# Optimization experiments

Measured on AMD Instinct MI355X. Metric: run time of the kernel, lower is better.

The kernel has to match this reference:

```python
import jax, jax.numpy as jnp
import numpy as np

B, S, DM1, DM2, DK, DV = 8, 2048, 768, 768, 64, 64
EPS = 1e-5


def setup_inputs() -> dict:
    key = jax.random.key(0)
    ks = jax.random.split(key, 8)
    s1 = 1.0 / np.sqrt(DM1)
    s2 = 1.0 / np.sqrt(DM2)
    return {
        "x_1": jax.random.normal(ks[0], (B, S, DM1), jnp.float32),
        "x_2": jax.random.normal(ks[1], (B, S, DM2), jnp.float32),
        "Wq": jax.random.uniform(ks[2], (DM1, DK), jnp.float32, -s1, s1),
        "bq": jnp.zeros((DK,), jnp.float32),
        "Wk": jax.random.uniform(ks[3], (DM2, DK), jnp.float32, -s2, s2),
        "bk": jnp.zeros((DK,), jnp.float32),
        "Wv": jax.random.uniform(ks[4], (DM2, DV), jnp.float32, -s2, s2),
        "bv": jnp.zeros((DV,), jnp.float32),
        "gamma": jnp.ones((DV,), jnp.float32),
        "beta": jnp.zeros((DV,), jnp.float32),
    }


def reference(x_1, x_2, Wq, bq, Wk, bk, Wv, bv, gamma, beta):
    q = jnp.einsum("bsd,dk->bsk", x_1, Wq) + bq            # [B,S,DK]
    k = jnp.einsum("bsd,dk->bsk", x_2, Wk) + bk            # [B,S,DK]
    v = jnp.einsum("bsd,dv->bsv", x_2, Wv) + bv            # [B,S,DV]
    scores = jnp.einsum("bqk,bsk->bqs", q, k) / jnp.sqrt(jnp.float32(DK))
    w = jax.nn.softmax(scores, axis=-1)                    # [B,S,S]
    # reverse-weight transform (reverse=True)
    dim = w.shape[1]
    w = (1.0 - w) / (dim - 1)
    attn = jnp.einsum("bqs,bsv->bqv", w, v)                # [B,S,DV]
    mu = jnp.mean(attn, axis=-1, keepdims=True)
    var = jnp.var(attn, axis=-1, keepdims=True)
    out = (attn - mu) * jax.lax.rsqrt(var + EPS) * gamma + beta
    return out
```

## Files before the change

kernel.cpp:

```cpp
#include <hip/hip_runtime.h>
#include <hip/hip_bf16.h>

#define BATCH 8
#define SEQ   2048
#define DM    768
#define DD    64
#define BS (BATCH * SEQ)
#define SCALEQ 0.1803369380478f

typedef __bf16 bf16x8 __attribute__((ext_vector_type(8)));
typedef float  f32x4  __attribute__((ext_vector_type(4)));
typedef short  short8 __attribute__((ext_vector_type(8)));
typedef short  short4v __attribute__((ext_vector_type(4)));

#define MFMA16(a, b, c) __builtin_amdgcn_mfma_f32_16x16x32_bf16((a), (b), (c), 0, 0, 0)

__device__ __forceinline__ short f2bf(float x) {
    unsigned u = __builtin_bit_cast(unsigned, x);
    u = (u + 0x7fffu + ((u >> 16) & 1u)) >> 16;
    return (short)u;
}
__device__ __forceinline__ float bf2f(short s) {
    unsigned u = ((unsigned)(unsigned short)s) << 16;
    return __builtin_bit_cast(float, u);
}
__device__ __forceinline__ bf16x8 cvt8(float4 a, float4 b) {
    bf16x8 r;
    r[0] = (__bf16)a.x; r[1] = (__bf16)a.y; r[2] = (__bf16)a.z; r[3] = (__bf16)a.w;
    r[4] = (__bf16)b.x; r[5] = (__bf16)b.y; r[6] = (__bf16)b.z; r[7] = (__bf16)b.w;
    return r;
}

__global__ void prep_w_kernel(const float* __restrict__ Wq, const float* __restrict__ Wk,
                              const float* __restrict__ Wv, short* __restrict__ Wt,
                              float* __restrict__ C) {
    int idx = blockIdx.x * 256 + threadIdx.x;
    if (idx < BATCH * DD) C[idx] = 0.f;
    if (idx >= 3 * DM * DD) return;
    int m = idx / (DM * DD);
    int r = (idx % (DM * DD)) / DD;
    int c = idx % DD;
    const float* W = (m == 0) ? Wq : (m == 1) ? Wk : Wv;
    float scale = (m == 0) ? SCALEQ : 1.0f;
    Wt[m * DM * DD + c * DM + r] = f2bf(W[r * DD + c] * scale);
}

__global__ __launch_bounds__(256, 2) void proj_kernel(
        const float* __restrict__ x1, const float* __restrict__ x2,
        const short* __restrict__ Wt,
        const float* __restrict__ bq, const float* __restrict__ bk,
        const float* __restrict__ bv,
        short* __restrict__ Qs, short* __restrict__ Kb, short* __restrict__ Vtb,
        float* __restrict__ C) {
    const int tid = threadIdx.x, wave = tid >> 6, lane = tid & 63;
    const int quad = lane >> 4, l15 = lane & 15;
    const int kv = blockIdx.x & 1;
    const int r0 = (blockIdx.x >> 1) * 64;
    const float* x = kv ? x2 : x1;
    const short* W0 = Wt + (kv ? (size_t)(DM * DD) : 0);
    const short* W1 = Wt + 2 * (size_t)(DM * DD);

    const float* xp = x + (size_t)(r0 + wave * 16 + l15) * DM + quad * 8;
    const short* wp0[4];
    const short* wp1[4];
#pragma unroll
    for (int tn = 0; tn < 4; tn++) {
        wp0[tn] = W0 + (size_t)(tn * 16 + l15) * DM + quad * 8;
        wp1[tn] = W1 + (size_t)(tn * 16 + l15) * DM + quad * 8;
    }

    f32x4 acc0[4] = {}, acc1[4] = {};

    if (!kv) {
#pragma unroll
        for (int st = 0; st < 24; st++) {
            const int k0 = st * 32;
            float4 a = *(const float4*)(xp + k0);
            float4 b = *(const float4*)(xp + k0 + 4);
            bf16x8 af = cvt8(a, b);
#pragma unroll
            for (int tn = 0; tn < 4; tn++)
                acc0[tn] = MFMA16(af, *(const bf16x8*)(wp0[tn] + k0), acc0[tn]);
        }
#pragma unroll
        for (int tn = 0; tn < 4; tn++) {
            int v = tn * 16 + l15;
            float bb = bq[v] * SCALEQ;
#pragma unroll
            for (int r = 0; r < 4; r++)
                Qs[(size_t)(r0 + wave * 16 + quad * 4 + r) * DD + v] = f2bf(acc0[tn][r] + bb);
        }
    } else {
#pragma unroll
        for (int st = 0; st < 24; st++) {
            const int k0 = st * 32;
            float4 a = *(const float4*)(xp + k0);
            float4 b = *(const float4*)(xp + k0 + 4);
            bf16x8 af = cvt8(a, b);
#pragma unroll
            for (int tn = 0; tn < 4; tn++) {
                acc0[tn] = MFMA16(af, *(const bf16x8*)(wp0[tn] + k0), acc0[tn]);
                acc1[tn] = MFMA16(af, *(const bf16x8*)(wp1[tn] + k0), acc1[tn]);
            }
        }
#pragma unroll
        for (int tn = 0; tn < 4; tn++) {
            int v = tn * 16 + l15;
            float bb = bk[v];
#pragma unroll
            for (int r = 0; r < 4; r++)
                Kb[(size_t)(r0 + wave * 16 + quad * 4 + r) * DD + v] = f2bf(acc0[tn][r] + bb);
        }
        const int b = r0 / SEQ;
        const int sbase = (r0 % SEQ) + wave * 16 + quad * 4;
#pragma unroll
        for (int tn = 0; tn < 4; tn++) {
            int v = tn * 16 + l15;
            float bb = bv[v];
            short4v pk;
            float cs = 0.f;
#pragma unroll
            for (int r = 0; r < 4; r++) {
                pk[r] = f2bf(acc1[tn][r] + bb);
                cs += bf2f(pk[r]);
            }
            *(short4v*)(Vtb + ((size_t)b * DD + v) * SEQ + sbase) = pk;
            cs += __shfl_xor(cs, 16);
            cs += __shfl_xor(cs, 32);
            if (quad == 0) atomicAdd(&C[b * DD + v], cs);
        }
    }
}

#define PBS 72
__global__ __launch_bounds__(256, 2) void flash_kernel(
        const short* __restrict__ Q, const short* __restrict__ K,
        const short* __restrict__ Vt,
        short* __restrict__ Yp, float* __restrict__ Dp) {
    __shared__ __align__(16) short pbuf[4][64 * PBS];
    __shared__ float dl[4][64];
    const int tid  = threadIdx.x;
    const int wave = tid >> 6, lane = tid & 63, quad = lane >> 4, l15 = lane & 15;
    const int blk = blockIdx.x;
    const int b = blk & 7, qt = (blk >> 3) & 31, half = blk >> 8;
    const int q0 = qt * 64;

    bf16x8 qf[4][2];
#pragma unroll
    for (int qn = 0; qn < 4; qn++)
#pragma unroll
        for (int kc = 0; kc < 2; kc++)
            qf[qn][kc] = *(const bf16x8*)(Q + ((size_t)(b * SEQ + q0 + qn * 16 + l15)) * DD
                                          + kc * 32 + quad * 8);

    const short* Kbp = K  + (size_t)b * SEQ * DD;
    const short* Vbp = Vt + (size_t)b * DD * SEQ;
    f32x4 y[4][4] = {};
    float den[4] = {0.f, 0.f, 0.f, 0.f};
    short* pw = &pbuf[wave][0];

    const int s_begin = half * 1024 + wave * 256;
    for (int s0 = s_begin; s0 < s_begin + 256; s0 += 64) {
#pragma unroll
        for (int tn = 0; tn < 4; tn++) {
            const short* kf = Kbp + (size_t)(s0 + tn * 16 + l15) * DD + quad * 8;
            bf16x8 ka0 = *(const bf16x8*)kf;
            bf16x8 ka1 = *(const bf16x8*)(kf + 32);
#pragma unroll
            for (int qn = 0; qn < 4; qn++) {
                f32x4 z = {0.f, 0.f, 0.f, 0.f};
                z = MFMA16(ka0, qf[qn][0], z);
                z = MFMA16(ka1, qf[qn][1], z);
                short4v pk;
#pragma unroll
                for (int r = 0; r < 4; r++) {
                    float p = __builtin_amdgcn_exp2f(z[r]);
                    den[qn] += p;
                    pk[r] = f2bf(p);
                }
                *(short4v*)&pw[(qn * 16 + l15) * PBS + tn * 16 + quad * 4] = pk;
            }
        }
#pragma unroll
        for (int kc = 0; kc < 2; kc++) {
            bf16x8 pB[4];
#pragma unroll
            for (int qn = 0; qn < 4; qn++)
                pB[qn] = *(const bf16x8*)&pw[(qn * 16 + l15) * PBS + kc * 32 + quad * 8];
#pragma unroll
            for (int vn = 0; vn < 4; vn++) {
                bf16x8 va = *(const bf16x8*)(Vbp + (size_t)(vn * 16 + l15) * SEQ
                                             + s0 + kc * 32 + quad * 8);
#pragma unroll
                for (int qn = 0; qn < 4; qn++)
                    y[qn][vn] = MFMA16(va, pB[qn], y[qn][vn]);
            }
        }
    }
#pragma unroll
    for (int qn = 0; qn < 4; qn++) {
        den[qn] += __shfl_xor(den[qn], 16);
        den[qn] += __shfl_xor(den[qn], 32);
    }
#pragma unroll
    for (int qn = 0; qn < 4; qn++) {
#pragma unroll
        for (int vn = 0; vn < 4; vn++) {
            short4v pk;
#pragma unroll
            for (int r = 0; r < 4; r++) pk[r] = f2bf(y[qn][vn][r]);
            *(short4v*)&pw[(qn * 16 + l15) * PBS + vn * 16 + quad * 4] = pk;
        }
        if (quad == 0) dl[wave][qn * 16 + l15] = den[qn];
    }
    __syncthreads();
    {
        const int q = wave * 16 + l15;
        float D = dl[0][q] + dl[1][q] + dl[2][q] + dl[3][q];
        float ys[16];
#pragma unroll
        for (int j = 0; j < 16; j++) ys[j] = 0.f;
#pragma unroll
        for (int u = 0; u < 4; u++) {
#pragma unroll
            for (int h = 0; h < 2; h++) {
                bf16x8 t = *(const bf16x8*)&pbuf[u][q * PBS + quad * 16 + h * 8];
#pragma unroll
                for (int j = 0; j < 8; j++) ys[h * 8 + j] += (float)t[j];
            }
        }
        const size_t row = (size_t)b * SEQ + q0 + q;
        short8 o0, o1;
#pragma unroll
        for (int j = 0; j < 8; j++) { o0[j] = f2bf(ys[j]); o1[j] = f2bf(ys[8 + j]); }
        short* yout = Yp + ((size_t)half * BS + row) * DD + quad * 16;
        *(short8*)yout = o0;
        *(short8*)(yout + 8) = o1;
        if (quad == 0) Dp[half * BS + row] = D;
    }
}

__global__ __launch_bounds__(256) void reduce_ln_kernel(
        const short* __restrict__ Yp, const float* __restrict__ Dp,
        const float* __restrict__ C, const float* __restrict__ gamma,
        const float* __restrict__ beta, float* __restrict__ out) {
    const int row = blockIdx.x * 4 + (threadIdx.x >> 6);
    const int v = threadIdx.x & 63;
    const int b = row >> 11;
    float Y = bf2f(Yp[(size_t)row * DD + v]) + bf2f(Yp[((size_t)BS + row) * DD + v]);
    float D = Dp[row] + Dp[BS + row];
    float attn = (C[b * DD + v] - Y / D) * (1.0f / (float)(SEQ - 1));
    float msum = attn, ssum = attn * attn;
#pragma unroll
    for (int m = 1; m < 64; m <<= 1) {
        msum += __shfl_xor(msum, m);
        ssum += __shfl_xor(ssum, m);
    }
    float mu = msum * (1.0f / 64.0f);
    float var = ssum * (1.0f / 64.0f) - mu * mu;
    float rs = rsqrtf(var + 1e-5f);
    out[(size_t)row * DD + v] = (attn - mu) * rs * gamma[v] + beta[v];
}

extern "C" void kernel_launch(void* const* d_in, const int* in_sizes, int n_in,
                              void* d_out, int out_size, void* d_ws, size_t ws_size,
                              hipStream_t stream) {
    const float* x1    = (const float*)d_in[0];
    const float* x2    = (const float*)d_in[1];
    const float* Wq    = (const float*)d_in[2];
    const float* bq    = (const float*)d_in[3];
    const float* Wk    = (const float*)d_in[4];
    const float* bk    = (const float*)d_in[5];
    const float* Wv    = (const float*)d_in[6];
    const float* bv    = (const float*)d_in[7];
    const float* gamma = (const float*)d_in[8];
    const float* beta  = (const float*)d_in[9];
    float* out = (float*)d_out;

    char* ws = (char*)d_ws;
    short* Qs  = (short*)(ws);
    short* Kbf = (short*)(ws + (2ull << 20));
    short* Vtb = (short*)(ws + (4ull << 20));
    short* Wt  = (short*)(ws + (6ull << 20));
    float* Cc  = (float*)(ws + (6ull << 20) + 3 * DM * DD * 2);
    short* Yp  = (short*)(ws + (7ull << 20));
    float* Dp  = (float*)(ws + (11ull << 20));

    prep_w_kernel<<<576, 256, 0, stream>>>(Wq, Wk, Wv, Wt, Cc);
    proj_kernel<<<512, 256, 0, stream>>>(x1, x2, Wt, bq, bk, bv, Qs, Kbf, Vtb, Cc);
    flash_kernel<<<512, 256, 0, stream>>>(Qs, Kbf, Vtb, Yp, Dp);
    reduce_ln_kernel<<<BS / 4, 256, 0, stream>>>(Yp, Dp, Cc, gamma, beta, out);
}
```

Measured before the change: 203.6 us.

## Restructure projection kernel: per-wave weight columns in registers, one output per block

The projection kernel is reorganized so each block computes exactly one of Q, K or V, giving 768 blocks instead of 512. Each wave keeps its 16 weight columns resident in registers across the whole reduction, and all four 16-row groups of x are streamed through with next-step prefetching. This replaces the previous layout, where every wave reloaded weights from global memory and K/V blocks did double work. The balanced blocks should even out the load, but x is now read by every wave of a block and K/V blocks read x2 twice, with higher register pressure from the 24 cached weight fragments.

```diff
diff --git a/kernel.cpp b/kernel.cpp
--- a/kernel.cpp
+++ b/kernel.cpp
@@ -54,81 +54,81 @@
         float* __restrict__ C) {
     const int tid = threadIdx.x, wave = tid >> 6, lane = tid & 63;
     const int quad = lane >> 4, l15 = lane & 15;
-    const int kv = blockIdx.x & 1;
-    const int r0 = (blockIdx.x >> 1) * 64;
-    const float* x = kv ? x2 : x1;
-    const short* W0 = Wt + (kv ? (size_t)(DM * DD) : 0);
-    const short* W1 = Wt + 2 * (size_t)(DM * DD);
-
-    const float* xp = x + (size_t)(r0 + wave * 16 + l15) * DM + quad * 8;
-    const short* wp0[4];
-    const short* wp1[4];
-#pragma unroll
-    for (int tn = 0; tn < 4; tn++) {
-        wp0[tn] = W0 + (size_t)(tn * 16 + l15) * DM + quad * 8;
-        wp1[tn] = W1 + (size_t)(tn * 16 + l15) * DM + quad * 8;
-    }
-
-    f32x4 acc0[4] = {}, acc1[4] = {};
-
-    if (!kv) {
-#pragma unroll
-        for (int st = 0; st < 24; st++) {
-            const int k0 = st * 32;
-            float4 a = *(const float4*)(xp + k0);
-            float4 b = *(const float4*)(xp + k0 + 4);
-            bf16x8 af = cvt8(a, b);
-#pragma unroll
-            for (int tn = 0; tn < 4; tn++)
-                acc0[tn] = MFMA16(af, *(const bf16x8*)(wp0[tn] + k0), acc0[tn]);
-        }
-#pragma unroll
-        for (int tn = 0; tn < 4; tn++) {
-            int v = tn * 16 + l15;
-            float bb = bq[v] * SCALEQ;
+    const int typ = blockIdx.x % 3;
+    const int g   = blockIdx.x / 3;
+    const int r0  = g * 64;
+    const float* x = (typ == 0) ? x1 : x2;
+    const int col = wave * 16 + l15;
+
+    const short* wp = Wt + ((size_t)typ * DD + col) * DM + quad * 8;
+    bf16x8 wreg[24];
+#pragma unroll
+    for (int st = 0; st < 24; st++)
+        wreg[st] = *(const bf16x8*)(wp + st * 32);
+
+    const float* xp = x + (size_t)(r0 + l15) * DM + quad * 8;
+
+    f32x4 acc[4] = {};
+    float4 ca[4], cb[4];
+#pragma unroll
+    for (int rn = 0; rn < 4; rn++) {
+        const float* p = xp + (size_t)(rn * 16) * DM;
+        ca[rn] = *(const float4*)(p);
+        cb[rn] = *(const float4*)(p + 4);
+    }
+#pragma unroll
+    for (int st = 0; st < 24; st++) {
+        float4 na[4], nb[4];
+        if (st + 1 < 24) {
+#pragma unroll
+            for (int rn = 0; rn < 4; rn++) {
+                const float* p = xp + (size_t)(rn * 16) * DM + (st + 1) * 32;
+                na[rn] = *(const float4*)(p);
+                nb[rn] = *(const float4*)(p + 4);
+            }
+        }
+#pragma unroll
+        for (int rn = 0; rn < 4; rn++) {
+            bf16x8 af = cvt8(ca[rn], cb[rn]);
+            acc[rn] = MFMA16(af, wreg[st], acc[rn]);
+        }
+#pragma unroll
+        for (int rn = 0; rn < 4; rn++) { ca[rn] = na[rn]; cb[rn] = nb[rn]; }
+    }
+
+    if (typ == 0) {
+        float bb = bq[col] * SCALEQ;
+#pragma unroll
+        for (int rn = 0; rn < 4; rn++)
 #pragma unroll
             for (int r = 0; r < 4; r++)
-                Qs[(size_t)(r0 + wave * 16 + quad * 4 + r) * DD + v] = f2bf(acc0[tn][r] + bb);
-        }
+                Qs[(size_t)(r0 + rn * 16 + quad * 4 + r) * DD + col] = f2bf(acc[rn][r] + bb);
+    } else if (typ == 1) {
+        float bb = bk[col];
+#pragma unroll
+        for (int rn = 0; rn < 4; rn++)
+#pragma unroll
+            for (int r = 0; r < 4; r++)
+                Kb[(size_t)(r0 + rn * 16 + quad * 4 + r) * DD + col] = f2bf(acc[rn][r] + bb);
     } else {
-#pragma unroll
-        for (int st = 0; st < 24; st++) {
-            const int k0 = st * 32;
-            float4 a = *(const float4*)(xp + k0);
-            float4 b = *(const float4*)(xp + k0 + 4);
-            bf16x8 af = cvt8(a, b);
-#pragma unroll
-            for (int tn = 0; tn < 4; tn++) {
-                acc0[tn] = MFMA16(af, *(const bf16x8*)(wp0[tn] + k0), acc0[tn]);
-                acc1[tn] = MFMA16(af, *(const bf16x8*)(wp1[tn] + k0), acc1[tn]);
-            }
-        }
-#pragma unroll
-        for (int tn = 0; tn < 4; tn++) {
-            int v = tn * 16 + l15;
-            float bb = bk[v];
-#pragma unroll
-            for (int r = 0; r < 4; r++)
-                Kb[(size_t)(r0 + wave * 16 + quad * 4 + r) * DD + v] = f2bf(acc0[tn][r] + bb);
-        }
-        const int b = r0 / SEQ;
-        const int sbase = (r0 % SEQ) + wave * 16 + quad * 4;
-#pragma unroll
-        for (int tn = 0; tn < 4; tn++) {
-            int v = tn * 16 + l15;
-            float bb = bv[v];
+        const int b  = r0 >> 11;
+        const int sb = r0 & 2047;
+        float bb = bv[col];
+        short* vout = Vtb + ((size_t)b * DD + col) * SEQ + sb;
+        float cs = 0.f;
+#pragma unroll
+        for (int rn = 0; rn < 4; rn++) {
             short4v pk;
-            float cs = 0.f;
 #pragma unroll
             for (int r = 0; r < 4; r++) {
-                pk[r] = f2bf(acc1[tn][r] + bb);
+                pk[r] = f2bf(acc[rn][r] + bb);
                 cs += bf2f(pk[r]);
             }
-            *(short4v*)(Vtb + ((size_t)b * DD + v) * SEQ + sbase) = pk;
-            cs += __shfl_xor(cs, 16);
-            cs += __shfl_xor(cs, 32);
-            if (quad == 0) atomicAdd(&C[b * DD + v], cs);
-        }
+            *(short4v*)(vout + rn * 16 + quad * 4) = pk;
+        }
+        cs += __shfl_xor(cs, 16);
+        cs += __shfl_xor(cs, 32);
+        if (quad == 0) atomicAdd(&C[b * DD + col], cs);
     }
 }
 
@@ -287,7 +287,7 @@
     float* Dp  = (float*)(ws + (11ull << 20));
 
     prep_w_kernel<<<576, 256, 0, stream>>>(Wq, Wk, Wv, Wt, Cc);
-    proj_kernel<<<512, 256, 0, stream>>>(x1, x2, Wt, bq, bk, bv, Qs, Kbf, Vtb, Cc);
+    proj_kernel<<<768, 256, 0, stream>>>(x1, x2, Wt, bq, bk, bv, Qs, Kbf, Vtb, Cc);
     flash_kernel<<<512, 256, 0, stream>>>(Qs, Kbf, Vtb, Yp, Dp);
     reduce_ln_kernel<<<BS / 4, 256, 0, stream>>>(Yp, Dp, Cc, gamma, beta, out);
 }
```

After: 212.6 us. 4.4% more time.

## Stage projection inputs and weights through double-buffered LDS via global_load_lds

Applied to the files above, without the earlier changes.

The projection GEMM used to read x and the bf16 weights straight from global memory into registers, with each wave loading the weight tiles on its own. It now uses direct global-to-LDS async loads into a double buffer, with an XOR swizzle on the x tile, so the next K-slice can prefetch while MFMAs run on the current one. Weights loaded into LDS are shared by all four waves, which cuts redundant global traffic. In exchange the loop now has a __syncthreads per K-step, the 24-step loop is no longer unrolled, and LDS use grows, which could lower occupancy.

```diff
diff --git a/kernel.cpp b/kernel.cpp
--- a/kernel.cpp
+++ b/kernel.cpp
@@ -29,6 +29,11 @@
     r[0] = (__bf16)a.x; r[1] = (__bf16)a.y; r[2] = (__bf16)a.z; r[3] = (__bf16)a.w;
     r[4] = (__bf16)b.x; r[5] = (__bf16)b.y; r[6] = (__bf16)b.z; r[7] = (__bf16)b.w;
     return r;
+}
+__device__ __forceinline__ void gld16(const void* g, void* l) {
+    __builtin_amdgcn_global_load_lds(
+        (const __attribute__((address_space(1))) void*)g,
+        (__attribute__((address_space(3))) void*)l, 16, 0, 0);
 }
 
 __global__ void prep_w_kernel(const float* __restrict__ Wq, const float* __restrict__ Wk,
@@ -52,36 +57,59 @@
         const float* __restrict__ bv,
         short* __restrict__ Qs, short* __restrict__ Kb, short* __restrict__ Vtb,
         float* __restrict__ C) {
+    __shared__ __align__(16) float als[2][64 * 32];
+    __shared__ __align__(16) short wls[2][2][2048];
     const int tid = threadIdx.x, wave = tid >> 6, lane = tid & 63;
     const int quad = lane >> 4, l15 = lane & 15;
     const int kv = blockIdx.x & 1;
     const int r0 = (blockIdx.x >> 1) * 64;
     const float* x = kv ? x2 : x1;
-    const short* W0 = Wt + (kv ? (size_t)(DM * DD) : 0);
-    const short* W1 = Wt + 2 * (size_t)(DM * DD);
-
-    const float* xp = x + (size_t)(r0 + wave * 16 + l15) * DM + quad * 8;
-    const short* wp0[4];
-    const short* wp1[4];
-#pragma unroll
-    for (int tn = 0; tn < 4; tn++) {
-        wp0[tn] = W0 + (size_t)(tn * 16 + l15) * DM + quad * 8;
-        wp1[tn] = W1 + (size_t)(tn * 16 + l15) * DM + quad * 8;
-    }
+    const int m0 = kv ? 1 : 0;
+
+    const int sg = wave * 2;
+    const int arow0 = sg * 8 + (lane >> 3);
+    const int aswz = ((lane & 7) ^ ((lane >> 3) & 7)) * 4;
+    const float* asrc0 = x + (size_t)(r0 + arow0) * DM + aswz;
+    const float* asrc1 = asrc0 + (size_t)8 * DM;
+    const short* wsrc0 = Wt + (size_t)(m0 * DD + lane) * DM + wave * 8;
+    const short* wsrc1 = Wt + (size_t)(2  * DD + lane) * DM + wave * 8;
 
     f32x4 acc0[4] = {}, acc1[4] = {};
 
+    gld16(asrc0, &als[0][sg * 256]);
+    gld16(asrc1, &als[0][(sg + 1) * 256]);
+    gld16(wsrc0, &wls[0][0][wave * 512]);
+    if (kv) gld16(wsrc1, &wls[0][1][wave * 512]);
+    __syncthreads();
+
+    const int arow = wave * 16 + l15;
+    const int s0 = (((quad * 2) ^ (l15 & 7))) * 4;
+    const int s1 = (((quad * 2 + 1) ^ (l15 & 7))) * 4;
+
+    for (int p = 0; p < 24; p++) {
+        const int cur = p & 1;
+        if (p + 1 < 24) {
+            gld16(asrc0 + (p + 1) * 32, &als[cur ^ 1][sg * 256]);
+            gld16(asrc1 + (p + 1) * 32, &als[cur ^ 1][(sg + 1) * 256]);
+            gld16(wsrc0 + (p + 1) * 32, &wls[cur ^ 1][0][wave * 512]);
+            if (kv) gld16(wsrc1 + (p + 1) * 32, &wls[cur ^ 1][1][wave * 512]);
+        }
+        float4 a0 = *(const float4*)&als[cur][arow * 32 + s0];
+        float4 a1 = *(const float4*)&als[cur][arow * 32 + s1];
+        bf16x8 af = cvt8(a0, a1);
+#pragma unroll
+        for (int tn = 0; tn < 4; tn++) {
+            bf16x8 w0 = *(const bf16x8*)&wls[cur][0][(quad * 64 + tn * 16 + l15) * 8];
+            acc0[tn] = MFMA16(af, w0, acc0[tn]);
+            if (kv) {
+                bf16x8 w1 = *(const bf16x8*)&wls[cur][1][(quad * 64 + tn * 16 + l15) * 8];
+                acc1[tn] = MFMA16(af, w1, acc1[tn]);
+            }
+        }
+        __syncthreads();
+    }
+
     if (!kv) {
-#pragma unroll
-        for (int st = 0; st < 24; st++) {
-            const int k0 = st * 32;
-            float4 a = *(const float4*)(xp + k0);
-            float4 b = *(const float4*)(xp + k0 + 4);
-            bf16x8 af = cvt8(a, b);
-#pragma unroll
-            for (int tn = 0; tn < 4; tn++)
-                acc0[tn] = MFMA16(af, *(const bf16x8*)(wp0[tn] + k0), acc0[tn]);
-        }
 #pragma unroll
         for (int tn = 0; tn < 4; tn++) {
             int v = tn * 16 + l15;
@@ -91,18 +119,6 @@
                 Qs[(size_t)(r0 + wave * 16 + quad * 4 + r) * DD + v] = f2bf(acc0[tn][r] + bb);
         }
     } else {
-#pragma unroll
-        for (int st = 0; st < 24; st++) {
-            const int k0 = st * 32;
-            float4 a = *(const float4*)(xp + k0);
-            float4 b = *(const float4*)(xp + k0 + 4);
-            bf16x8 af = cvt8(a, b);
-#pragma unroll
-            for (int tn = 0; tn < 4; tn++) {
-                acc0[tn] = MFMA16(af, *(const bf16x8*)(wp0[tn] + k0), acc0[tn]);
-                acc1[tn] = MFMA16(af, *(const bf16x8*)(wp1[tn] + k0), acc1[tn]);
-            }
-        }
 #pragma unroll
         for (int tn = 0; tn < 4; tn++) {
             int v = tn * 16 + l15;
```

Measured after the change: 181.6 us. 10.8% less time.
